# Performance work log

Measured on AMD Instinct MI355X. Metric: run time of the kernel, lower is better.

Reference implementation:

```python
import jax, jax.numpy as jnp
import numpy as np

B, S, H = 32, 256, 256
D = 2 * H          # BiLSTM output dim (hidden_dim*2)
F = 1024           # total fragment count across the batch
T = 5              # tagset size


def setup_inputs() -> dict:
    key = jax.random.key(0)
    ks = jax.random.split(key, 9)
    en_output = jax.random.normal(ks[0], (B, S, D), jnp.float32)
    # descending lengths, first sentence defines seq_length = S
    lengths = jnp.sort(jax.random.randint(ks[1], (B,), S // 2, S + 1))[::-1]
    lengths = lengths.at[0].set(S)
    frag_b = jax.random.randint(ks[2], (F,), 0, B)
    frag_s = jax.random.randint(ks[3], (F,), 0, S // 2 - 8)
    width = jax.random.randint(ks[4], (F,), 1, 8)
    frag_e = frag_s + width  # end exclusive, always <= lengths[frag_b]
    att_w = jax.random.normal(ks[5], (3 * D, D), jnp.float32) / np.float32(np.sqrt(3 * D))
    att_b = jax.random.normal(ks[6], (3 * D,), jnp.float32) * 0.01
    tag_w = jax.random.normal(ks[7], (T, 4 * D), jnp.float32) / np.float32(np.sqrt(4 * D))
    tag_b = jax.random.normal(ks[8], (T,), jnp.float32) * 0.01
    return {"en_output": en_output, "lengths": lengths, "frag_b": frag_b,
            "frag_s": frag_s, "frag_e": frag_e, "att_w": att_w, "att_b": att_b,
            "tag_w": tag_w, "tag_b": tag_b}


def reference(en_output, lengths, frag_b, frag_s, frag_e, att_w, att_b, tag_w, tag_b):
    Fn = frag_b.shape[0]
    Bn, Sn, Dn = en_output.shape
    dtype = en_output.dtype
    pos = jnp.arange(Sn)                                            # [S]
    in_span = (pos[None, :] >= frag_s[:, None]) & (pos[None, :] < frag_e[:, None])  # [F,S]
    memory = en_output[frag_b]                                      # [F,S,D] gather per fragment
    # word_state = sum of hidden states over the span (segment-sum via mask)
    word_state = jnp.einsum('fs,fsd->fd', in_span.astype(dtype), memory)
    l_word = en_output[frag_b, frag_s]                              # [F,D]
    r_word = en_output[frag_b, frag_e - 1]                          # [F,D]
    span = jnp.concatenate([l_word, word_state, r_word], axis=-1)   # [F,3D]
    # attention mask: the span itself and all padding positions are masked out
    att_mask = in_span | (pos[None, :] >= lengths[frag_b][:, None])  # [F,S]
    seq_len = lengths[0]
    # position distance (int), then position weight 1 - dist/seq_len
    pos_dis = jnp.where(pos[None, :] < frag_s[:, None], frag_s[:, None] - pos[None, :],
                jnp.where(pos[None, :] >= frag_e[:, None], pos[None, :] - frag_e[:, None] + 1,
                          seq_len)).astype(dtype)
    pos_weight = 1.0 - pos_dis / seq_len.astype(dtype)
    final = pos_weight[:, :, None] * memory                         # [F,S,D]
    # att(final) @ span == final @ (att_w.T span) + att_b.span ; att_w is [3D, D] (torch Linear weight)
    v = span @ att_w                                                # [F,D]
    c = span @ att_b                                                # [F]
    scores = jnp.tanh(jnp.einsum('fsd,fd->fs', final, v) + c[:, None])
    scores = jnp.where(att_mask, jnp.asarray(-1e4, dtype), scores)
    att = jax.nn.softmax(scores, axis=1)                            # [F,S]
    mix = jnp.einsum('fs,fsd->fd', att, final)                      # [F,D]
    mix_state = jnp.concatenate([span, mix], axis=-1)               # [F,4D]
    logits = mix_state @ tag_w.T + tag_b                            # [F,T]
    return jax.nn.log_softmax(logits, axis=1)
```

## Files before the change

### kernel.cpp

```cpp
#include <hip/hip_runtime.h>
#include <math.h>

#define BB 32
#define SS 256
#define DD 512
#define FF 1024
#define TT 5
#define K3 1536
#define K4 2048
#define GK 1536
#define SK 4
#define KCH (GK / SK)

__device__ __forceinline__ float wave_reduce_sum(float x) {
#pragma unroll
  for (int o = 32; o > 0; o >>= 1) x += __shfl_xor(x, o);
  return x;
}

__global__ __launch_bounds__(128)
void span_kernel(const float* __restrict__ en, const int* __restrict__ fb,
                 const int* __restrict__ fs, const int* __restrict__ fe,
                 const float* __restrict__ att_b,
                 float* __restrict__ span, float* __restrict__ cvec)
{
  int f = blockIdx.x;
  int t = threadIdx.x;
  int b = fb[f], s = fs[f], e = fe[f];
  const float* base = en + (size_t)b * SS * DD;
  int d0 = t * 4;
  float4 lw = *(const float4*)(base + (size_t)s * DD + d0);
  float4 rw = *(const float4*)(base + (size_t)(e - 1) * DD + d0);
  float4 wsum = make_float4(0.f, 0.f, 0.f, 0.f);
  for (int p = s; p < e; ++p) {
    float4 m = *(const float4*)(base + (size_t)p * DD + d0);
    wsum.x += m.x; wsum.y += m.y; wsum.z += m.z; wsum.w += m.w;
  }
  float* sp = span + (size_t)f * K3;
  *(float4*)(sp + d0) = lw;
  *(float4*)(sp + DD + d0) = wsum;
  *(float4*)(sp + 2 * DD + d0) = rw;
  float4 a0 = *(const float4*)(att_b + d0);
  float4 a1 = *(const float4*)(att_b + DD + d0);
  float4 a2 = *(const float4*)(att_b + 2 * DD + d0);
  float part = lw.x*a0.x + lw.y*a0.y + lw.z*a0.z + lw.w*a0.w
             + wsum.x*a1.x + wsum.y*a1.y + wsum.z*a1.z + wsum.w*a1.w
             + rw.x*a2.x + rw.y*a2.y + rw.z*a2.z + rw.w*a2.w;
  part = wave_reduce_sum(part);
  __shared__ float red[2];
  if ((t & 63) == 0) red[t >> 6] = part;
  __syncthreads();
  if (t == 0) cvec[f] = red[0] + red[1];
}

__global__ __launch_bounds__(256)
void gemm_v(const float* __restrict__ A,
            const float* __restrict__ Bw,
            float* __restrict__ Cpart)
{
  const int BM = 32, BN = 64, BK = 16;
  __shared__ float As[BK][BM + 2];
  __shared__ float Bs[BK][BN + 4];
  int t = threadIdx.x;
  int n0 = blockIdx.x * BN;
  int m0 = blockIdx.y * BM;
  int sk = blockIdx.z;
  int kbase = sk * KCH;

  int ar = t >> 3;
  int ac = (t & 7) * 2;
  int br = t >> 4;
  int bc = (t & 15) * 4;
  int tm = (t >> 4) * 2;
  int tn = (t & 15) * 4;

  float acc[2][4] = {};

  for (int k0 = kbase; k0 < kbase + KCH; k0 += BK) {
    float2 av = *(const float2*)(A + (size_t)(m0 + ar) * GK + k0 + ac);
    float4 bv = *(const float4*)(Bw + (size_t)(k0 + br) * DD + n0 + bc);
    __syncthreads();
    As[ac][ar] = av.x;
    As[ac + 1][ar] = av.y;
    *(float4*)(&Bs[br][bc]) = bv;
    __syncthreads();
#pragma unroll
    for (int k = 0; k < BK; ++k) {
      float a0 = As[k][tm], a1 = As[k][tm + 1];
      float4 b = *(float4*)(&Bs[k][tn]);
      acc[0][0] += a0 * b.x; acc[0][1] += a0 * b.y; acc[0][2] += a0 * b.z; acc[0][3] += a0 * b.w;
      acc[1][0] += a1 * b.x; acc[1][1] += a1 * b.y; acc[1][2] += a1 * b.z; acc[1][3] += a1 * b.w;
    }
  }
  float* Cp = Cpart + (size_t)sk * FF * DD;
#pragma unroll
  for (int i = 0; i < 2; ++i) {
    *(float4*)(Cp + (size_t)(m0 + tm + i) * DD + n0 + tn) =
        make_float4(acc[i][0], acc[i][1], acc[i][2], acc[i][3]);
  }
}

__global__ __launch_bounds__(256)
void frag_kernel(const float* __restrict__ en, const int* __restrict__ lengths,
                 const int* __restrict__ fb, const int* __restrict__ fs,
                 const int* __restrict__ fe,
                 const float* __restrict__ span, const float* __restrict__ cvec,
                 const float* __restrict__ vpart,
                 const float* __restrict__ tag_w, const float* __restrict__ tag_b,
                 float* __restrict__ out)
{
  __shared__ float v_lds[DD];
  __shared__ float buf[4][DD];
  __shared__ float mstate[4][2];
  __shared__ float mix_lds[DD];
  __shared__ float pl[4 * TT];
  __shared__ float l5[TT];

  int f = blockIdx.x;
  int t = threadIdx.x;
  int lane = t & 63, wv = t >> 6;
  int b = fb[f], s = fs[f], e = fe[f];
  int lenb = lengths[b];
  float seqlen = (float)lengths[0];
  float c = cvec[f];
  const float* mem = en + (size_t)b * SS * DD;

  if (t < 128) {
    float4 v0 = *(const float4*)(vpart + (size_t)f * DD + t * 4);
    float4 v1 = *(const float4*)(vpart + (size_t)FF * DD + (size_t)f * DD + t * 4);
    float4 v2 = *(const float4*)(vpart + 2 * (size_t)FF * DD + (size_t)f * DD + t * 4);
    float4 v3 = *(const float4*)(vpart + 3 * (size_t)FF * DD + (size_t)f * DD + t * 4);
    *(float4*)(v_lds + t * 4) = make_float4(v0.x + v1.x + v2.x + v3.x,
                                            v0.y + v1.y + v2.y + v3.y,
                                            v0.z + v1.z + v2.z + v3.z,
                                            v0.w + v1.w + v2.w + v3.w);
  }
  __syncthreads();

  float4 va = *(float4*)(v_lds + lane * 8);
  float4 vb = *(float4*)(v_lds + lane * 8 + 4);
  float m = -1e30f, ssum = 0.f;
  float am[8] = {0.f, 0.f, 0.f, 0.f, 0.f, 0.f, 0.f, 0.f};

  for (int i = 0; i < 64; ++i) {
    int p = wv * 64 + i;
    const float* row = mem + (size_t)p * DD + lane * 8;
    float4 r0 = *(const float4*)(row);
    float4 r1 = *(const float4*)(row + 4);
    float d = r0.x*va.x + r0.y*va.y + r0.z*va.z + r0.w*va.w
            + r1.x*vb.x + r1.y*vb.y + r1.z*vb.z + r1.w*vb.w;
    d = wave_reduce_sum(d);
    bool mask = (p >= s && p < e) || (p >= lenb);
    if (!mask) {
      float dis = (p < s) ? (float)(s - p) : (float)(p - e + 1);
      float pw = 1.f - dis / seqlen;
      float sc = tanhf(pw * d + c);
      if (sc > m) {
        float scale = __expf(m - sc);
        ssum *= scale;
#pragma unroll
        for (int j = 0; j < 8; ++j) am[j] *= scale;
        m = sc;
      }
      float u = __expf(sc - m);
      ssum += u;
      float upw = u * pw;
      am[0] += upw * r0.x; am[1] += upw * r0.y; am[2] += upw * r0.z; am[3] += upw * r0.w;
      am[4] += upw * r1.x; am[5] += upw * r1.y; am[6] += upw * r1.z; am[7] += upw * r1.w;
    }
  }
  if (lane == 0) { mstate[wv][0] = m; mstate[wv][1] = ssum; }
  __syncthreads();
  float M = fmaxf(fmaxf(mstate[0][0], mstate[1][0]), fmaxf(mstate[2][0], mstate[3][0]));
  float S = mstate[0][1] * __expf(mstate[0][0] - M)
          + mstate[1][1] * __expf(mstate[1][0] - M)
          + mstate[2][1] * __expf(mstate[2][0] - M)
          + mstate[3][1] * __expf(mstate[3][0] - M);
  float ew = __expf(m - M);
  {
    float4 s0 = make_float4(am[0] * ew, am[1] * ew, am[2] * ew, am[3] * ew);
    float4 s1 = make_float4(am[4] * ew, am[5] * ew, am[6] * ew, am[7] * ew);
    *(float4*)(&buf[wv][lane * 8]) = s0;
    *(float4*)(&buf[wv][lane * 8 + 4]) = s1;
  }
  __syncthreads();
  {
    int d0 = t * 2;
    float inv = 1.f / S;
    mix_lds[d0]     = (buf[0][d0] + buf[1][d0] + buf[2][d0] + buf[3][d0]) * inv;
    mix_lds[d0 + 1] = (buf[0][d0 + 1] + buf[1][d0 + 1] + buf[2][d0 + 1] + buf[3][d0 + 1]) * inv;
  }
  __syncthreads();

  float vals[8];
  int idx = t * 8;
  if (idx < K3) {
    const float* sp = span + (size_t)f * K3 + idx;
    float4 x0 = *(const float4*)(sp);
    float4 x1 = *(const float4*)(sp + 4);
    vals[0]=x0.x; vals[1]=x0.y; vals[2]=x0.z; vals[3]=x0.w;
    vals[4]=x1.x; vals[5]=x1.y; vals[6]=x1.z; vals[7]=x1.w;
  } else {
#pragma unroll
    for (int j = 0; j < 8; ++j) vals[j] = mix_lds[idx - K3 + j];
  }
  float acc5[TT];
#pragma unroll
  for (int tg = 0; tg < TT; ++tg) {
    const float* twr = tag_w + (size_t)tg * K4 + idx;
    float a = 0.f;
#pragma unroll
    for (int j = 0; j < 8; ++j) a += vals[j] * twr[j];
    acc5[tg] = wave_reduce_sum(a);
  }
  if (lane == 0) {
#pragma unroll
    for (int tg = 0; tg < TT; ++tg) pl[wv * TT + tg] = acc5[tg];
  }
  __syncthreads();
  if (t < TT) {
    l5[t] = pl[t] + pl[TT + t] + pl[2 * TT + t] + pl[3 * TT + t] + tag_b[t];
  }
  __syncthreads();
  if (t == 0) {
    float mm = l5[0];
#pragma unroll
    for (int j = 1; j < TT; ++j) mm = fmaxf(mm, l5[j]);
    float se = 0.f;
#pragma unroll
    for (int j = 0; j < TT; ++j) se += __expf(l5[j] - mm);
    float lse = mm + logf(se);
#pragma unroll
    for (int j = 0; j < TT; ++j) out[(size_t)f * TT + j] = l5[j] - lse;
  }
}

extern "C" void kernel_launch(void* const* d_in, const int* in_sizes, int n_in,
                              void* d_out, int out_size, void* d_ws, size_t ws_size,
                              hipStream_t stream) {
  const float* en      = (const float*)d_in[0];
  const int*   lengths = (const int*)d_in[1];
  const int*   frag_b  = (const int*)d_in[2];
  const int*   frag_s  = (const int*)d_in[3];
  const int*   frag_e  = (const int*)d_in[4];
  const float* att_w   = (const float*)d_in[5];
  const float* att_b   = (const float*)d_in[6];
  const float* tag_w   = (const float*)d_in[7];
  const float* tag_b   = (const float*)d_in[8];
  float* out = (float*)d_out;

  float* span  = (float*)d_ws;
  float* cvec  = span + (size_t)FF * K3;
  float* vpart = cvec + FF;

  span_kernel<<<FF, 128, 0, stream>>>(en, frag_b, frag_s, frag_e, att_b, span, cvec);
  gemm_v<<<dim3(8, 32, SK), 256, 0, stream>>>(span, att_w, vpart);
  frag_kernel<<<FF, 256, 0, stream>>>(en, lengths, frag_b, frag_s, frag_e,
                                      span, cvec, vpart, tag_w, tag_b, out);
}
```

Before: 163.1 us.

## Bucket fragments by batch for L2 locality, batch loads and shuffles, use fast tanh

```diff
diff --git a/kernel.cpp b/kernel.cpp
--- a/kernel.cpp
+++ b/kernel.cpp
@@ -16,6 +16,31 @@
 #pragma unroll
   for (int o = 32; o > 0; o >>= 1) x += __shfl_xor(x, o);
   return x;
+}
+
+__device__ __forceinline__ float fast_tanh(float x) {
+  float ax = fabsf(x);
+  float t = __expf(-2.f * ax);
+  float r = (1.f - t) / (1.f + t);
+  return x < 0.f ? -r : r;
+}
+
+__global__ __launch_bounds__(1024)
+void bucket_kernel(const int* __restrict__ fb, int* __restrict__ order) {
+  __shared__ int cnt[BB];
+  __shared__ int start[BB];
+  int t = threadIdx.x;
+  if (t < BB) cnt[t] = 0;
+  __syncthreads();
+  int b = fb[t];
+  int r = atomicAdd(&cnt[b], 1);
+  __syncthreads();
+  if (t == 0) {
+    int acc = 0;
+    for (int i = 0; i < BB; ++i) { start[i] = acc; acc += cnt[i]; }
+  }
+  __syncthreads();
+  order[start[b] + r] = t;
 }
 
 __global__ __launch_bounds__(128)
@@ -107,6 +132,7 @@
                  const float* __restrict__ span, const float* __restrict__ cvec,
                  const float* __restrict__ vpart,
                  const float* __restrict__ tag_w, const float* __restrict__ tag_b,
+                 const int* __restrict__ order,
                  float* __restrict__ out)
 {
   __shared__ float v_lds[DD];
@@ -116,7 +142,8 @@
   __shared__ float pl[4 * TT];
   __shared__ float l5[TT];
 
-  int f = blockIdx.x;
+  int bid = blockIdx.x;
+  int f = order[(bid & 7) * (FF / 8) + (bid >> 3)];
   int t = threadIdx.x;
   int lane = t & 63, wv = t >> 6;
   int b = fb[f], s = fs[f], e = fe[f];
@@ -142,31 +169,44 @@
   float m = -1e30f, ssum = 0.f;
   float am[8] = {0.f, 0.f, 0.f, 0.f, 0.f, 0.f, 0.f, 0.f};
 
-  for (int i = 0; i < 64; ++i) {
-    int p = wv * 64 + i;
-    const float* row = mem + (size_t)p * DD + lane * 8;
-    float4 r0 = *(const float4*)(row);
-    float4 r1 = *(const float4*)(row + 4);
-    float d = r0.x*va.x + r0.y*va.y + r0.z*va.z + r0.w*va.w
-            + r1.x*vb.x + r1.y*vb.y + r1.z*vb.z + r1.w*vb.w;
-    d = wave_reduce_sum(d);
-    bool mask = (p >= s && p < e) || (p >= lenb);
-    if (!mask) {
-      float dis = (p < s) ? (float)(s - p) : (float)(p - e + 1);
-      float pw = 1.f - dis / seqlen;
-      float sc = tanhf(pw * d + c);
-      if (sc > m) {
-        float scale = __expf(m - sc);
-        ssum *= scale;
-#pragma unroll
-        for (int j = 0; j < 8; ++j) am[j] *= scale;
-        m = sc;
+  for (int i0 = 0; i0 < 64; i0 += 8) {
+    float4 R0[8], R1[8];
+    float d8[8];
+#pragma unroll
+    for (int k = 0; k < 8; ++k) {
+      int p = wv * 64 + i0 + k;
+      const float* row = mem + (size_t)p * DD + lane * 8;
+      R0[k] = *(const float4*)(row);
+      R1[k] = *(const float4*)(row + 4);
+      d8[k] = R0[k].x*va.x + R0[k].y*va.y + R0[k].z*va.z + R0[k].w*va.w
+            + R1[k].x*vb.x + R1[k].y*vb.y + R1[k].z*vb.z + R1[k].w*vb.w;
+    }
+#pragma unroll
+    for (int o = 32; o > 0; o >>= 1) {
+#pragma unroll
+      for (int k = 0; k < 8; ++k) d8[k] += __shfl_xor(d8[k], o);
+    }
+#pragma unroll
+    for (int k = 0; k < 8; ++k) {
+      int p = wv * 64 + i0 + k;
+      bool mask = (p >= s && p < e) || (p >= lenb);
+      if (!mask) {
+        float dis = (p < s) ? (float)(s - p) : (float)(p - e + 1);
+        float pw = 1.f - dis / seqlen;
+        float sc = fast_tanh(pw * d8[k] + c);
+        if (sc > m) {
+          float scale = __expf(m - sc);
+          ssum *= scale;
+#pragma unroll
+          for (int j = 0; j < 8; ++j) am[j] *= scale;
+          m = sc;
+        }
+        float u = __expf(sc - m);
+        ssum += u;
+        float upw = u * pw;
+        am[0] += upw * R0[k].x; am[1] += upw * R0[k].y; am[2] += upw * R0[k].z; am[3] += upw * R0[k].w;
+        am[4] += upw * R1[k].x; am[5] += upw * R1[k].y; am[6] += upw * R1[k].z; am[7] += upw * R1[k].w;
       }
-      float u = __expf(sc - m);
-      ssum += u;
-      float upw = u * pw;
-      am[0] += upw * r0.x; am[1] += upw * r0.y; am[2] += upw * r0.z; am[3] += upw * r0.w;
-      am[4] += upw * r1.x; am[5] += upw * r1.y; am[6] += upw * r1.z; am[7] += upw * r1.w;
     }
   }
   if (lane == 0) { mstate[wv][0] = m; mstate[wv][1] = ssum; }
@@ -252,9 +292,11 @@
   float* span  = (float*)d_ws;
   float* cvec  = span + (size_t)FF * K3;
   float* vpart = cvec + FF;
-
+  int*   order = (int*)(vpart + (size_t)SK * FF * DD);
+
+  bucket_kernel<<<1, FF, 0, stream>>>(frag_b, order);
   span_kernel<<<FF, 128, 0, stream>>>(en, frag_b, frag_s, frag_e, att_b, span, cvec);
   gemm_v<<<dim3(8, 32, SK), 256, 0, stream>>>(span, att_w, vpart);
   frag_kernel<<<FF, 256, 0, stream>>>(en, lengths, frag_b, frag_s, frag_e,
-                                      span, cvec, vpart, tag_w, tag_b, out);
-}
+                                      span, cvec, vpart, tag_w, tag_b, order, out);
+}
```

After: 159.4 us. -2.3%, faster.
